# Kernel tuning notes

Measured on AMD Instinct MI355X. Metric: run time of the kernel, lower is better.

## Reference

```python
import jax, jax.numpy as jnp
import numpy as np

B, N, M, D_IN, D_OUT, H = 4, 2048, 2048, 512, 512, 8
HD = D_OUT // H
LN_EPS = 1e-5


def setup_inputs() -> dict:
    key = jax.random.key(0)
    ks = jax.random.split(key, 10)
    query = jax.random.normal(ks[0], (B, N, D_IN), dtype=jnp.float32)
    kee = jax.random.normal(ks[1], (B, M, D_IN), dtype=jnp.float32)
    val = jax.random.normal(ks[2], (B, M, D_IN), dtype=jnp.float32)
    mask = jax.random.randint(ks[3], (B, N, M), 0, 2, dtype=jnp.int32)
    # xavier_uniform with gain 1/sqrt(2): limit = gain * sqrt(6/(fan_in+fan_out))
    lim = (1.0 / np.sqrt(2.0)) * np.sqrt(6.0 / (D_IN + D_OUT))
    WQ = jax.random.uniform(ks[4], (D_OUT, D_IN), jnp.float32, -lim, lim)
    WK = jax.random.uniform(ks[5], (D_OUT, D_IN), jnp.float32, -lim, lim)
    WV = jax.random.uniform(ks[6], (D_OUT, D_IN), jnp.float32, -lim, lim)
    limO = (1.0 / np.sqrt(2.0)) * np.sqrt(6.0 / (D_OUT + D_OUT))
    WO = jax.random.uniform(ks[7], (D_OUT, D_OUT), jnp.float32, -limO, limO)
    bO = jnp.zeros((D_OUT,), jnp.float32)
    gamma = jnp.ones((D_OUT,), jnp.float32)
    beta = jnp.zeros((D_OUT,), jnp.float32)
    return {"query": query, "key": kee, "value": val, "mask": mask,
            "WQ": WQ, "WK": WK, "WV": WV, "WO": WO, "bO": bO,
            "gamma": gamma, "beta": beta}


def reference(query, key, value, mask, WQ, WK, WV, WO, bO, gamma, beta):
    scale = jnp.float32(1.0 / np.sqrt(HD))
    # project and split heads: [B, H, S, HD]
    Q = (query @ WQ.T).reshape(B, N, H, HD).transpose(0, 2, 1, 3)
    K = (key @ WK.T).reshape(B, M, H, HD).transpose(0, 2, 1, 3)
    V = (value @ WV.T).reshape(B, M, H, HD).transpose(0, 2, 1, 3)
    attn = jnp.einsum('bhnd,bhmd->bhnm', Q, K) * scale
    attn = jnp.where(mask[:, None, :, :] == 0, -jnp.inf, attn)
    attn = jax.nn.softmax(attn, axis=-1)  # dropout is identity in eval
    out = jnp.einsum('bhnm,bhmd->bhnd', attn, V)
    out = out.transpose(0, 2, 1, 3).reshape(B, N, D_OUT)
    out = out @ WO.T + bO
    x = out + query  # residual_proj is Identity (input_dim == output_dim)
    mu = jnp.mean(x, axis=-1, keepdims=True)
    var = jnp.var(x, axis=-1, keepdims=True)
    return (x - mu) * jax.lax.rsqrt(var + LN_EPS) * gamma + beta
```

## Files before the change

### kernel.cpp

```cpp
#include <hip/hip_runtime.h>
#include <stdint.h>

#define B_   4
#define N_   2048
#define M_   2048
#define DIN  512
#define DOUT 512
#define H_   8
#define HD_  64
#define ROWS (B_ * N_)

typedef __attribute__((ext_vector_type(8))) short bf16x8;
typedef __attribute__((ext_vector_type(4))) float f32x4;
typedef unsigned short u16;
typedef unsigned int   u32;

__device__ __forceinline__ u16 f2bf(float x) {
  union { float f; u32 u; } v; v.f = x;
  u32 r = (v.u + 0x7FFFu + ((v.u >> 16) & 1u)) >> 16;
  return (u16)r;
}

__device__ __forceinline__ void gld16(u16* lds, const u16* g) {
  __builtin_amdgcn_global_load_lds((const __attribute__((address_space(1))) u32*)g,
                                   (__attribute__((address_space(3))) u32*)lds, 16, 0, 0);
}

__global__ __launch_bounds__(256) void k_convert3(
    const float* __restrict__ a0, const float* __restrict__ a1, const float* __restrict__ a2,
    u16* __restrict__ d0, u16* __restrict__ d1, u16* __restrict__ d2)
{
  int t = blockIdx.x * 256 + threadIdx.x;
  int seg = t >> 19;
  int i = (t & 524287) << 3;
  const float* s = seg == 0 ? a0 : seg == 1 ? a1 : a2;
  u16* d = seg == 0 ? d0 : seg == 1 ? d1 : d2;
  f32x4 x = *(const f32x4*)(s + i);
  f32x4 y = *(const f32x4*)(s + i + 4);
  bf16x8 r;
  r[0] = (short)f2bf(x[0]); r[1] = (short)f2bf(x[1]);
  r[2] = (short)f2bf(x[2]); r[3] = (short)f2bf(x[3]);
  r[4] = (short)f2bf(y[0]); r[5] = (short)f2bf(y[1]);
  r[6] = (short)f2bf(y[2]); r[7] = (short)f2bf(y[3]);
  *(bf16x8*)(d + i) = r;
}

__global__ __launch_bounds__(256) void k_convertw(
    const float* __restrict__ a0, const float* __restrict__ a1,
    const float* __restrict__ a2, const float* __restrict__ a3,
    u16* __restrict__ d0, u16* __restrict__ d1, u16* __restrict__ d2, u16* __restrict__ d3)
{
  int t = blockIdx.x * 256 + threadIdx.x;
  int seg = t >> 15;
  int i = (t & 32767) << 3;
  const float* s = seg == 0 ? a0 : seg == 1 ? a1 : seg == 2 ? a2 : a3;
  u16* d = seg == 0 ? d0 : seg == 1 ? d1 : seg == 2 ? d2 : d3;
  f32x4 x = *(const f32x4*)(s + i);
  f32x4 y = *(const f32x4*)(s + i + 4);
  bf16x8 r;
  r[0] = (short)f2bf(x[0]); r[1] = (short)f2bf(x[1]);
  r[2] = (short)f2bf(x[2]); r[3] = (short)f2bf(x[3]);
  r[4] = (short)f2bf(y[0]); r[5] = (short)f2bf(y[1]);
  r[6] = (short)f2bf(y[2]); r[7] = (short)f2bf(y[3]);
  *(bf16x8*)(d + i) = r;
}

__global__ __launch_bounds__(256) void k_maskpack(const int* __restrict__ mask, u32* __restrict__ bits)
{
  int lane = threadIdx.x & 63;
  int gw = (blockIdx.x * 256 + threadIdx.x) >> 6;
  #pragma unroll 4
  for (int it = 0; it < 32; ++it) {
    long pos = ((long)(it * 8192 + gw)) * 64 + lane;
    int v = mask[pos];
    unsigned long long bal = __ballot(v != 0);
    if ((lane & 31) == 0) bits[pos >> 5] = (u32)(bal >> lane);
  }
}

__global__ __launch_bounds__(256) void k_gemm_qkv(
    const u16* __restrict__ Aq, const u16* __restrict__ Ak, const u16* __restrict__ Av,
    const u16* __restrict__ Wq, const u16* __restrict__ Wk, const u16* __restrict__ Wv,
    u16* __restrict__ Qo, u16* __restrict__ Ko, u16* __restrict__ Vt)
{
  __shared__ __align__(16) u16 At[128 * 64];
  __shared__ __align__(16) u16 Bt[128 * 64];
  const int z = blockIdx.z;
  const u16* A = z == 0 ? Aq : z == 1 ? Ak : Av;
  const u16* W = z == 0 ? Wq : z == 1 ? Wk : Wv;
  const int bm = blockIdx.y, bn = blockIdx.x;
  const int t = threadIdx.x, l = t & 63;
  const int w = t >> 6, wr = w >> 1, wc = w & 1;
  const int l15 = l & 15, lg = l >> 4;
  f32x4 acc[4][4] = {};
  const u16* ga = A + (size_t)(bm * 128 + (t >> 3)) * DIN + (t & 7) * 8;
  const u16* gb = W + (size_t)(bn * 128 + (t >> 3)) * DIN + (t & 7) * 8;
  u16* la = &At[t * 8];
  u16* lb = &Bt[t * 8];
  for (int kt = 0; kt < 8; ++kt) {
    const int k0 = kt * 64;
    #pragma unroll
    for (int s2 = 0; s2 < 4; ++s2) {
      gld16(la + s2 * 2048, ga + (size_t)s2 * 32 * DIN + k0);
      gld16(lb + s2 * 2048, gb + (size_t)s2 * 32 * DIN + k0);
    }
    __syncthreads();
    bf16x8 af[4][2], bfr[4][2];
    #pragma unroll
    for (int mi = 0; mi < 4; ++mi)
      #pragma unroll
      for (int c = 0; c < 2; ++c)
        af[mi][c] = *(const bf16x8*)&At[(wr * 64 + mi * 16 + l15) * 64 + c * 32 + lg * 8];
    #pragma unroll
    for (int ni = 0; ni < 4; ++ni)
      #pragma unroll
      for (int c = 0; c < 2; ++c)
        bfr[ni][c] = *(const bf16x8*)&Bt[(wc * 64 + ni * 16 + l15) * 64 + c * 32 + lg * 8];
    #pragma unroll
    for (int mi = 0; mi < 4; ++mi)
      #pragma unroll
      for (int ni = 0; ni < 4; ++ni) {
        acc[mi][ni] = __builtin_amdgcn_mfma_f32_16x16x32_bf16(af[mi][0], bfr[ni][0], acc[mi][ni], 0, 0, 0);
        acc[mi][ni] = __builtin_amdgcn_mfma_f32_16x16x32_bf16(af[mi][1], bfr[ni][1], acc[mi][ni], 0, 0, 0);
      }
    __syncthreads();
  }
  if (z < 2) {
    u16* C = z == 0 ? Qo : Ko;
    const float scl = z == 0 ? 0.125f : 1.0f;
    #pragma unroll
    for (int mi = 0; mi < 4; ++mi)
      #pragma unroll
      for (int ni = 0; ni < 4; ++ni) {
        const int m = bm * 128 + wr * 64 + mi * 16 + lg * 4;
        const int o = bn * 128 + wc * 64 + ni * 16 + l15;
        #pragma unroll
        for (int r = 0; r < 4; ++r)
          C[(size_t)(m + r) * DOUT + o] = f2bf(acc[mi][ni][r] * scl);
      }
  } else {
    #pragma unroll
    for (int mi = 0; mi < 4; ++mi)
      #pragma unroll
      for (int ni = 0; ni < 4; ++ni) {
        #pragma unroll
        for (int r = 0; r < 4; ++r) {
          const int m = bm * 128 + wr * 64 + mi * 16 + lg * 4 + r;
          const int o = bn * 128 + wc * 64 + ni * 16 + l15;
          const int bb = m >> 11, s = m & 2047;
          Vt[(size_t)(bb * 512 + o) * M_ + s] = f2bf(acc[mi][ni][r]);
        }
      }
  }
}

__global__ __launch_bounds__(256) void k_attn(
    const u16* __restrict__ Qp, const u16* __restrict__ Kp, const u16* __restrict__ Vt,
    const u32* __restrict__ mbits, u16* __restrict__ AO)
{
  __shared__ __align__(16) u16 KT[2][64 * 64];
  __shared__ __align__(16) u16 VT[2][64 * 64];
  const int qt = blockIdx.x, bh = blockIdx.y;
  const int b = bh >> 3, h = bh & 7;
  const int t = threadIdx.x, l = t & 63, w = t >> 6;
  const int l15 = l & 15, lg = l >> 4;

  const int srow = t >> 3;
  const int scol8 = t & 7;
  const int scol = (scol8 ^ (srow & 7)) * 8;
  const int kpr = (srow >> 5) * 32 + (((srow >> 4) & 1) * 4) + (((srow & 15) >> 2) * 8) + (srow & 3);
  const u16* gK = Kp + (size_t)(b * N_ + kpr) * DOUT + h * HD_ + scol;
  const u16* gV = Vt + (size_t)(b * 512 + h * HD_ + srow) * M_ + scol;

  const size_t qglob = (size_t)(b * N_ + qt * 64 + w * 16 + l15);
  const bf16x8 qb0 = *(const bf16x8*)&Qp[qglob * DOUT + h * HD_ + lg * 8];
  const bf16x8 qb1 = *(const bf16x8*)&Qp[qglob * DOUT + h * HD_ + 32 + lg * 8];
  const size_t mrowbase = ((size_t)(b * N_) + qt * 64 + w * 16 + l15) * (M_ / 32);

  f32x4 o0 = {}, o1 = {}, o2 = {}, o3 = {};
  float lsum = 0.f;

  #define STAGE(buf_, m0_) do {                                   \
    const u16* gk_ = gK + (size_t)(m0_) * DOUT;                   \
    const u16* gv_ = gV + (m0_);                                  \
    u16* lk_ = &KT[buf_][t * 8];                                  \
    u16* lv_ = &VT[buf_][t * 8];                                  \
    gld16(lk_, gk_);                                              \
    gld16(lk_ + 2048, gk_ + (size_t)32 * DOUT);                   \
    gld16(lv_, gv_);                                              \
    gld16(lv_ + 2048, gv_ + (size_t)32 * M_);                     \
  } while (0)

  STAGE(0, 0);
  __syncthreads();

  for (int it = 0; it < 32; ++it) {
    const int buf = it & 1;
    const int m0 = it * 64;
    if (it + 1 < 32) STAGE(buf ^ 1, m0 + 64);

    const u32 mw0 = mbits[mrowbase + (m0 >> 5)];
    const u32 mw1 = mbits[mrowbase + (m0 >> 5) + 1];

    const u16* Kb = KT[buf];
    const u16* Vb = VT[buf];

    f32x4 s_[2][2];
    #pragma unroll
    for (int kb = 0; kb < 2; ++kb)
      #pragma unroll
      for (int u = 0; u < 2; ++u) {
        const int row = kb * 32 + u * 16 + l15;
        const bf16x8 a0 = *(const bf16x8*)&Kb[row * 64 + ((lg ^ (row & 7)) * 8)];
        const bf16x8 a1 = *(const bf16x8*)&Kb[row * 64 + (((4 + lg) ^ (row & 7)) * 8)];
        f32x4 z = {};
        z = __builtin_amdgcn_mfma_f32_16x16x32_bf16(a0, qb0, z, 0, 0, 0);
        z = __builtin_amdgcn_mfma_f32_16x16x32_bf16(a1, qb1, z, 0, 0, 0);
        s_[kb][u] = z;
      }

    u32 pk_[2][4];
    #pragma unroll
    for (int kb = 0; kb < 2; ++kb) {
      const u32 mw = kb ? mw1 : mw0;
      float pv[8];
      #pragma unroll
      for (int u = 0; u < 2; ++u)
        #pragma unroll
        for (int r = 0; r < 4; ++r) {
          const int bit = lg * 8 + u * 4 + r;
          float p = __expf(s_[kb][u][r]);
          p = ((mw >> bit) & 1u) ? p : 0.f;
          lsum += p;
          pv[u * 4 + r] = p;
        }
      #pragma unroll
      for (int j = 0; j < 4; ++j) {
        u32 rr;
        asm("v_cvt_pk_bf16_f32 %0, %1, %2" : "=v"(rr) : "v"(pv[2 * j]), "v"(pv[2 * j + 1]));
        pk_[kb][j] = rr;
      }
    }

    union { u32 u[4]; bf16x8 v; } pa0, pa1;
    pa0.u[0] = pk_[0][0]; pa0.u[1] = pk_[0][1]; pa0.u[2] = pk_[0][2]; pa0.u[3] = pk_[0][3];
    pa1.u[0] = pk_[1][0]; pa1.u[1] = pk_[1][1]; pa1.u[2] = pk_[1][2]; pa1.u[3] = pk_[1][3];
    #pragma unroll
    for (int nd = 0; nd < 4; ++nd) {
      const int vrow = nd * 16 + l15;
      const bf16x8 vb0 = *(const bf16x8*)&Vb[vrow * 64 + ((lg ^ (l15 & 7)) * 8)];
      const bf16x8 vb1 = *(const bf16x8*)&Vb[vrow * 64 + (((4 + lg) ^ (l15 & 7)) * 8)];
      f32x4* oo = nd == 0 ? &o0 : nd == 1 ? &o1 : nd == 2 ? &o2 : &o3;
      *oo = __builtin_amdgcn_mfma_f32_16x16x32_bf16(pa0.v, vb0, *oo, 0, 0, 0);
      *oo = __builtin_amdgcn_mfma_f32_16x16x32_bf16(pa1.v, vb1, *oo, 0, 0, 0);
    }
    __syncthreads();
  }

  lsum += __shfl_xor(lsum, 16);
  lsum += __shfl_xor(lsum, 32);
  const float rin = lsum > 0.f ? 1.f / lsum : 0.f;
  float rq[4];
  #pragma unroll
  for (int r = 0; r < 4; ++r) rq[r] = __shfl(rin, lg * 4 + r);
  f32x4* ovec[4] = { &o0, &o1, &o2, &o3 };
  #pragma unroll
  for (int nd = 0; nd < 4; ++nd)
    #pragma unroll
    for (int r = 0; r < 4; ++r) {
      const int q = qt * 64 + w * 16 + lg * 4 + r;
      AO[((size_t)(b * N_ + q)) * DOUT + h * HD_ + nd * 16 + l15] = f2bf((*ovec[nd])[r] * rq[r]);
    }
  #undef STAGE
}

__global__ __launch_bounds__(256) void k_gemm_out(
    const u16* __restrict__ A, const u16* __restrict__ W,
    const float* __restrict__ bO, const float* __restrict__ query,
    float* __restrict__ X)
{
  __shared__ __align__(16) u16 At[128 * 64];
  __shared__ __align__(16) u16 Bt[128 * 64];
  const int bm = blockIdx.y, bn = blockIdx.x;
  const int t = threadIdx.x, l = t & 63;
  const int w = t >> 6, wr = w >> 1, wc = w & 1;
  const int l15 = l & 15, lg = l >> 4;
  f32x4 acc[4][4] = {};
  const u16* ga = A + (size_t)(bm * 128 + (t >> 3)) * DOUT + (t & 7) * 8;
  const u16* gb = W + (size_t)(bn * 128 + (t >> 3)) * DOUT + (t & 7) * 8;
  u16* la = &At[t * 8];
  u16* lb = &Bt[t * 8];
  for (int kt = 0; kt < 8; ++kt) {
    const int k0 = kt * 64;
    #pragma unroll
    for (int s2 = 0; s2 < 4; ++s2) {
      gld16(la + s2 * 2048, ga + (size_t)s2 * 32 * DOUT + k0);
      gld16(lb + s2 * 2048, gb + (size_t)s2 * 32 * DOUT + k0);
    }
    __syncthreads();
    bf16x8 af[4][2], bfr[4][2];
    #pragma unroll
    for (int mi = 0; mi < 4; ++mi)
      #pragma unroll
      for (int c = 0; c < 2; ++c)
        af[mi][c] = *(const bf16x8*)&At[(wr * 64 + mi * 16 + l15) * 64 + c * 32 + lg * 8];
    #pragma unroll
    for (int ni = 0; ni < 4; ++ni)
      #pragma unroll
      for (int c = 0; c < 2; ++c)
        bfr[ni][c] = *(const bf16x8*)&Bt[(wc * 64 + ni * 16 + l15) * 64 + c * 32 + lg * 8];
    #pragma unroll
    for (int mi = 0; mi < 4; ++mi)
      #pragma unroll
      for (int ni = 0; ni < 4; ++ni) {
        acc[mi][ni] = __builtin_amdgcn_mfma_f32_16x16x32_bf16(af[mi][0], bfr[ni][0], acc[mi][ni], 0, 0, 0);
        acc[mi][ni] = __builtin_amdgcn_mfma_f32_16x16x32_bf16(af[mi][1], bfr[ni][1], acc[mi][ni], 0, 0, 0);
      }
    __syncthreads();
  }
  #pragma unroll
  for (int mi = 0; mi < 4; ++mi)
    #pragma unroll
    for (int ni = 0; ni < 4; ++ni) {
      const int m = bm * 128 + wr * 64 + mi * 16 + lg * 4;
      const int o = bn * 128 + wc * 64 + ni * 16 + l15;
      const float bo = bO[o];
      #pragma unroll
      for (int r = 0; r < 4; ++r) {
        const size_t idx = (size_t)(m + r) * DOUT + o;
        X[idx] = acc[mi][ni][r] + bo + query[idx];
      }
    }
}

__global__ __launch_bounds__(256) void k_ln(
    const float* __restrict__ X, const float* __restrict__ gamma,
    const float* __restrict__ beta, float* __restrict__ out)
{
  const int w = threadIdx.x >> 6, l = threadIdx.x & 63;
  const int row = blockIdx.x * 4 + w;
  const float* x = X + (size_t)row * DOUT + l * 8;
  f32x4 a = *(const f32x4*)(x);
  f32x4 b = *(const f32x4*)(x + 4);
  float s = a[0] + a[1] + a[2] + a[3] + b[0] + b[1] + b[2] + b[3];
  float q = a[0]*a[0] + a[1]*a[1] + a[2]*a[2] + a[3]*a[3]
          + b[0]*b[0] + b[1]*b[1] + b[2]*b[2] + b[3]*b[3];
  #pragma unroll
  for (int m = 1; m < 64; m <<= 1) { s += __shfl_xor(s, m); q += __shfl_xor(q, m); }
  const float mean = s * (1.f / 512.f);
  const float var = q * (1.f / 512.f) - mean * mean;
  const float rstd = rsqrtf(var + 1e-5f);
  f32x4 g1 = *(const f32x4*)(gamma + l * 8);
  f32x4 g2 = *(const f32x4*)(gamma + l * 8 + 4);
  f32x4 e1 = *(const f32x4*)(beta + l * 8);
  f32x4 e2 = *(const f32x4*)(beta + l * 8 + 4);
  f32x4 r1, r2;
  #pragma unroll
  for (int i = 0; i < 4; ++i) {
    r1[i] = (a[i] - mean) * rstd * g1[i] + e1[i];
    r2[i] = (b[i] - mean) * rstd * g2[i] + e2[i];
  }
  float* op = out + (size_t)row * DOUT + l * 8;
  *(f32x4*)(op) = r1;
  *(f32x4*)(op + 4) = r2;
}

extern "C" void kernel_launch(void* const* d_in, const int* in_sizes, int n_in,
                              void* d_out, int out_size, void* d_ws, size_t ws_size,
                              hipStream_t stream)
{
  const float* query = (const float*)d_in[0];
  const float* key   = (const float*)d_in[1];
  const float* value = (const float*)d_in[2];
  const int*   mask  = (const int*)d_in[3];
  const float* WQ    = (const float*)d_in[4];
  const float* WK    = (const float*)d_in[5];
  const float* WV    = (const float*)d_in[6];
  const float* WO    = (const float*)d_in[7];
  const float* bO    = (const float*)d_in[8];
  const float* gamma = (const float*)d_in[9];
  const float* beta  = (const float*)d_in[10];
  float* out = (float*)d_out;

  char* ws = (char*)d_ws;
  size_t off = 0;
  auto alloc = [&](size_t bytes) -> char* {
    char* p = ws + off;
    off += (bytes + 255) & ~(size_t)255;
    return p;
  };
  u16* qb  = (u16*)alloc((size_t)ROWS * DIN * 2);
  u16* kb  = (u16*)alloc((size_t)ROWS * DIN * 2);
  u16* vb  = (u16*)alloc((size_t)ROWS * DIN * 2);
  u16* wq  = (u16*)alloc((size_t)DOUT * DIN * 2);
  u16* wk  = (u16*)alloc((size_t)DOUT * DIN * 2);
  u16* wv  = (u16*)alloc((size_t)DOUT * DIN * 2);
  u16* wo  = (u16*)alloc((size_t)DOUT * DIN * 2);
  u16* Qp  = (u16*)alloc((size_t)ROWS * DOUT * 2);
  u16* Kp  = (u16*)alloc((size_t)ROWS * DOUT * 2);
  u16* Vt  = (u16*)alloc((size_t)ROWS * DOUT * 2);
  u32* mb  = (u32*)alloc((size_t)B_ * N_ * (M_ / 32) * 4);
  u16* AO  = (u16*)alloc((size_t)ROWS * DOUT * 2);
  float* X = (float*)alloc((size_t)ROWS * DOUT * 4);

  k_convert3 <<<6144, 256, 0, stream>>>(query, key, value, qb, kb, vb);
  k_convertw <<<512, 256, 0, stream>>>(WQ, WK, WV, WO, wq, wk, wv, wo);
  k_maskpack <<<2048, 256, 0, stream>>>(mask, mb);
  k_gemm_qkv <<<dim3(4, 64, 3), 256, 0, stream>>>(qb, kb, vb, wq, wk, wv, Qp, Kp, Vt);
  k_attn     <<<dim3(32, 32), 256, 0, stream>>>(Qp, Kp, Vt, mb, AO);
  k_gemm_out <<<dim3(4, 64), 256, 0, stream>>>(AO, wo, bO, query, X);
  k_ln       <<<2048, 256, 0, stream>>>(X, gamma, beta, out);
}
```

Baseline: 289.4 us.

## Read int mask directly in attention, merge conversions, double query rows per wave

Drops the separate mask bit-packing kernel. The attention kernel now reads the int32 mask straight from global memory and multiplies the probabilities by it. The two fp32-to-bf16 conversion kernels become a single launch. Each wave now handles 32 query rows instead of 16, so every K/V tile loaded into LDS is reused twice, and the grid is halved. The softmax scale folds in log2(e) so the kernel can use exp2, and row sums are computed with an MFMA against a ones vector instead of scalar adds and shuffles. In exchange, attention reads the full 4-byte-per-element mask (64 MB of mask traffic across all heads) instead of packed bits, and each wave needs more registers.

New measurement: 287.4 us. Within noise of the previous version (-0.7%).

```diff
diff --git a/kernel.cpp b/kernel.cpp
--- a/kernel.cpp
+++ b/kernel.cpp
@@ -15,6 +15,12 @@
 typedef unsigned short u16;
 typedef unsigned int   u32;
 
+#if __has_builtin(__builtin_amdgcn_exp2f)
+#define EXP2(x) __builtin_amdgcn_exp2f(x)
+#else
+#define EXP2(x) exp2f(x)
+#endif
+
 __device__ __forceinline__ u16 f2bf(float x) {
   union { float f; u32 u; } v; v.f = x;
   u32 r = (v.u + 0x7FFFu + ((v.u >> 16) & 1u)) >> 16;
@@ -26,15 +32,27 @@
                                    (__attribute__((address_space(3))) u32*)lds, 16, 0, 0);
 }
 
-__global__ __launch_bounds__(256) void k_convert3(
-    const float* __restrict__ a0, const float* __restrict__ a1, const float* __restrict__ a2,
-    u16* __restrict__ d0, u16* __restrict__ d1, u16* __restrict__ d2)
-{
-  int t = blockIdx.x * 256 + threadIdx.x;
-  int seg = t >> 19;
-  int i = (t & 524287) << 3;
-  const float* s = seg == 0 ? a0 : seg == 1 ? a1 : a2;
-  u16* d = seg == 0 ? d0 : seg == 1 ? d1 : d2;
+__global__ __launch_bounds__(256) void k_prep(
+    const float* __restrict__ q, const float* __restrict__ k, const float* __restrict__ v,
+    const float* __restrict__ wq_, const float* __restrict__ wk_,
+    const float* __restrict__ wv_, const float* __restrict__ wo_,
+    u16* __restrict__ qb, u16* __restrict__ kb, u16* __restrict__ vb,
+    u16* __restrict__ wqb, u16* __restrict__ wkb, u16* __restrict__ wvb, u16* __restrict__ wob)
+{
+  const int id = blockIdx.x;
+  const float* s; u16* d; size_t i;
+  if (id < 6144) {
+    const int seg = id >> 11;
+    s = seg == 0 ? q : seg == 1 ? k : v;
+    d = seg == 0 ? qb : seg == 1 ? kb : vb;
+    i = (size_t)(id & 2047) * 2048 + threadIdx.x * 8;
+  } else {
+    const int wid = id - 6144;
+    const int seg = wid >> 7;
+    s = seg == 0 ? wq_ : seg == 1 ? wk_ : seg == 2 ? wv_ : wo_;
+    d = seg == 0 ? wqb : seg == 1 ? wkb : seg == 2 ? wvb : wob;
+    i = (size_t)(wid & 127) * 2048 + threadIdx.x * 8;
+  }
   f32x4 x = *(const f32x4*)(s + i);
   f32x4 y = *(const f32x4*)(s + i + 4);
   bf16x8 r;
@@ -43,39 +61,6 @@
   r[4] = (short)f2bf(y[0]); r[5] = (short)f2bf(y[1]);
   r[6] = (short)f2bf(y[2]); r[7] = (short)f2bf(y[3]);
   *(bf16x8*)(d + i) = r;
-}
-
-__global__ __launch_bounds__(256) void k_convertw(
-    const float* __restrict__ a0, const float* __restrict__ a1,
-    const float* __restrict__ a2, const float* __restrict__ a3,
-    u16* __restrict__ d0, u16* __restrict__ d1, u16* __restrict__ d2, u16* __restrict__ d3)
-{
-  int t = blockIdx.x * 256 + threadIdx.x;
-  int seg = t >> 15;
-  int i = (t & 32767) << 3;
-  const float* s = seg == 0 ? a0 : seg == 1 ? a1 : seg == 2 ? a2 : a3;
-  u16* d = seg == 0 ? d0 : seg == 1 ? d1 : seg == 2 ? d2 : d3;
-  f32x4 x = *(const f32x4*)(s + i);
-  f32x4 y = *(const f32x4*)(s + i + 4);
-  bf16x8 r;
-  r[0] = (short)f2bf(x[0]); r[1] = (short)f2bf(x[1]);
-  r[2] = (short)f2bf(x[2]); r[3] = (short)f2bf(x[3]);
-  r[4] = (short)f2bf(y[0]); r[5] = (short)f2bf(y[1]);
-  r[6] = (short)f2bf(y[2]); r[7] = (short)f2bf(y[3]);
-  *(bf16x8*)(d + i) = r;
-}
-
-__global__ __launch_bounds__(256) void k_maskpack(const int* __restrict__ mask, u32* __restrict__ bits)
-{
-  int lane = threadIdx.x & 63;
-  int gw = (blockIdx.x * 256 + threadIdx.x) >> 6;
-  #pragma unroll 4
-  for (int it = 0; it < 32; ++it) {
-    long pos = ((long)(it * 8192 + gw)) * 64 + lane;
-    int v = mask[pos];
-    unsigned long long bal = __ballot(v != 0);
-    if ((lane & 31) == 0) bits[pos >> 5] = (u32)(bal >> lane);
-  }
 }
 
 __global__ __launch_bounds__(256) void k_gemm_qkv(
@@ -127,7 +112,7 @@
   }
   if (z < 2) {
     u16* C = z == 0 ? Qo : Ko;
-    const float scl = z == 0 ? 0.125f : 1.0f;
+    const float scl = z == 0 ? 0.18033688f : 1.0f;
     #pragma unroll
     for (int mi = 0; mi < 4; ++mi)
       #pragma unroll
@@ -156,7 +141,7 @@
 
 __global__ __launch_bounds__(256) void k_attn(
     const u16* __restrict__ Qp, const u16* __restrict__ Kp, const u16* __restrict__ Vt,
-    const u32* __restrict__ mbits, u16* __restrict__ AO)
+    const int* __restrict__ mask, u16* __restrict__ AO)
 {
   __shared__ __align__(16) u16 KT[2][64 * 64];
   __shared__ __align__(16) u16 VT[2][64 * 64];
@@ -172,13 +157,22 @@
   const u16* gK = Kp + (size_t)(b * N_ + kpr) * DOUT + h * HD_ + scol;
   const u16* gV = Vt + (size_t)(b * 512 + h * HD_ + srow) * M_ + scol;
 
-  const size_t qglob = (size_t)(b * N_ + qt * 64 + w * 16 + l15);
-  const bf16x8 qb0 = *(const bf16x8*)&Qp[qglob * DOUT + h * HD_ + lg * 8];
-  const bf16x8 qb1 = *(const bf16x8*)&Qp[qglob * DOUT + h * HD_ + 32 + lg * 8];
-  const size_t mrowbase = ((size_t)(b * N_) + qt * 64 + w * 16 + l15) * (M_ / 32);
-
-  f32x4 o0 = {}, o1 = {}, o2 = {}, o3 = {};
-  float lsum = 0.f;
+  const int qrow0 = qt * 128 + w * 32 + l15;
+  const bf16x8 qf[2][2] = {
+    { *(const bf16x8*)&Qp[((size_t)(b * N_) + qrow0) * DOUT + h * HD_ + lg * 8],
+      *(const bf16x8*)&Qp[((size_t)(b * N_) + qrow0) * DOUT + h * HD_ + 32 + lg * 8] },
+    { *(const bf16x8*)&Qp[((size_t)(b * N_) + qrow0 + 16) * DOUT + h * HD_ + lg * 8],
+      *(const bf16x8*)&Qp[((size_t)(b * N_) + qrow0 + 16) * DOUT + h * HD_ + 32 + lg * 8] } };
+
+  const int* mk[2] = { mask + ((size_t)(b * N_) + qrow0) * M_ + lg * 8,
+                       mask + ((size_t)(b * N_) + qrow0 + 16) * M_ + lg * 8 };
+
+  f32x4 o[2][4] = {};
+  f32x4 lacc[2] = {};
+
+  union U8 { u32 u[4]; bf16x8 v; };
+  U8 ones;
+  ones.u[0] = ones.u[1] = ones.u[2] = ones.u[3] = 0x3F803F80u;
 
   #define STAGE(buf_, m0_) do {                                   \
     const u16* gk_ = gK + (size_t)(m0_) * DOUT;                   \
@@ -199,78 +193,86 @@
     const int m0 = it * 64;
     if (it + 1 < 32) STAGE(buf ^ 1, m0 + 64);
 
-    const u32 mw0 = mbits[mrowbase + (m0 >> 5)];
-    const u32 mw1 = mbits[mrowbase + (m0 >> 5) + 1];
-
     const u16* Kb = KT[buf];
     const u16* Vb = VT[buf];
-
-    f32x4 s_[2][2];
+    const int xs = l15 & 7;
+
+    bf16x8 ka[2][2][2];
     #pragma unroll
     for (int kb = 0; kb < 2; ++kb)
       #pragma unroll
       for (int u = 0; u < 2; ++u) {
         const int row = kb * 32 + u * 16 + l15;
-        const bf16x8 a0 = *(const bf16x8*)&Kb[row * 64 + ((lg ^ (row & 7)) * 8)];
-        const bf16x8 a1 = *(const bf16x8*)&Kb[row * 64 + (((4 + lg) ^ (row & 7)) * 8)];
-        f32x4 z = {};
-        z = __builtin_amdgcn_mfma_f32_16x16x32_bf16(a0, qb0, z, 0, 0, 0);
-        z = __builtin_amdgcn_mfma_f32_16x16x32_bf16(a1, qb1, z, 0, 0, 0);
-        s_[kb][u] = z;
-      }
-
-    u32 pk_[2][4];
-    #pragma unroll
-    for (int kb = 0; kb < 2; ++kb) {
-      const u32 mw = kb ? mw1 : mw0;
-      float pv[8];
-      #pragma unroll
-      for (int u = 0; u < 2; ++u)
+        ka[kb][u][0] = *(const bf16x8*)&Kb[row * 64 + ((lg ^ xs) * 8)];
+        ka[kb][u][1] = *(const bf16x8*)&Kb[row * 64 + (((4 + lg) ^ xs) * 8)];
+      }
+
+    U8 pa[2][2];
+    #pragma unroll
+    for (int s = 0; s < 2; ++s) {
+      f32x4 sS[2][2];
+      #pragma unroll
+      for (int kb = 0; kb < 2; ++kb)
         #pragma unroll
-        for (int r = 0; r < 4; ++r) {
-          const int bit = lg * 8 + u * 4 + r;
-          float p = __expf(s_[kb][u][r]);
-          p = ((mw >> bit) & 1u) ? p : 0.f;
-          lsum += p;
-          pv[u * 4 + r] = p;
+        for (int u = 0; u < 2; ++u) {
+          f32x4 z = {};
+          z = __builtin_amdgcn_mfma_f32_16x16x32_bf16(ka[kb][u][0], qf[s][0], z, 0, 0, 0);
+          z = __builtin_amdgcn_mfma_f32_16x16x32_bf16(ka[kb][u][1], qf[s][1], z, 0, 0, 0);
+          sS[kb][u] = z;
         }
       #pragma unroll
-      for (int j = 0; j < 4; ++j) {
-        u32 rr;
-        asm("v_cvt_pk_bf16_f32 %0, %1, %2" : "=v"(rr) : "v"(pv[2 * j]), "v"(pv[2 * j + 1]));
-        pk_[kb][j] = rr;
-      }
-    }
-
-    union { u32 u[4]; bf16x8 v; } pa0, pa1;
-    pa0.u[0] = pk_[0][0]; pa0.u[1] = pk_[0][1]; pa0.u[2] = pk_[0][2]; pa0.u[3] = pk_[0][3];
-    pa1.u[0] = pk_[1][0]; pa1.u[1] = pk_[1][1]; pa1.u[2] = pk_[1][2]; pa1.u[3] = pk_[1][3];
+      for (int kb = 0; kb < 2; ++kb) {
+        const int4 ma  = *(const int4*)(mk[s] + m0 + kb * 32);
+        const int4 mb2 = *(const int4*)(mk[s] + m0 + kb * 32 + 4);
+        float e[8];
+        #pragma unroll
+        for (int u = 0; u < 2; ++u)
+          #pragma unroll
+          for (int r = 0; r < 4; ++r)
+            e[u * 4 + r] = EXP2(sS[kb][u][r]);
+        e[0] *= (float)ma.x;  e[1] *= (float)ma.y;  e[2] *= (float)ma.z;  e[3] *= (float)ma.w;
+        e[4] *= (float)mb2.x; e[5] *= (float)mb2.y; e[6] *= (float)mb2.z; e[7] *= (float)mb2.w;
+        #pragma unroll
+        for (int j = 0; j < 4; ++j) {
+          u32 rr;
+          asm("v_cvt_pk_bf16_f32 %0, %1, %2" : "=v"(rr) : "v"(e[2 * j]), "v"(e[2 * j + 1]));
+          pa[s][kb].u[j] = rr;
+        }
+      }
+      lacc[s] = __builtin_amdgcn_mfma_f32_16x16x32_bf16(pa[s][0].v, ones.v, lacc[s], 0, 0, 0);
+      lacc[s] = __builtin_amdgcn_mfma_f32_16x16x32_bf16(pa[s][1].v, ones.v, lacc[s], 0, 0, 0);
+    }
+
     #pragma unroll
     for (int nd = 0; nd < 4; ++nd) {
       const int vrow = nd * 16 + l15;
-      const bf16x8 vb0 = *(const bf16x8*)&Vb[vrow * 64 + ((lg ^ (l15 & 7)) * 8)];
-      const bf16x8 vb1 = *(const bf16x8*)&Vb[vrow * 64 + (((4 + lg) ^ (l15 & 7)) * 8)];
-      f32x4* oo = nd == 0 ? &o0 : nd == 1 ? &o1 : nd == 2 ? &o2 : &o3;
-      *oo = __builtin_amdgcn_mfma_f32_16x16x32_bf16(pa0.v, vb0, *oo, 0, 0, 0);
-      *oo = __builtin_amdgcn_mfma_f32_16x16x32_bf16(pa1.v, vb1, *oo, 0, 0, 0);
+      const bf16x8 vb0 = *(const bf16x8*)&Vb[vrow * 64 + ((lg ^ xs) * 8)];
+      const bf16x8 vb1 = *(const bf16x8*)&Vb[vrow * 64 + (((4 + lg) ^ xs) * 8)];
+      #pragma unroll
+      for (int s = 0; s < 2; ++s) {
+        o[s][nd] = __builtin_amdgcn_mfma_f32_16x16x32_bf16(pa[s][0].v, vb0, o[s][nd], 0, 0, 0);
+        o[s][nd] = __builtin_amdgcn_mfma_f32_16x16x32_bf16(pa[s][1].v, vb1, o[s][nd], 0, 0, 0);
+      }
     }
     __syncthreads();
   }
 
-  lsum += __shfl_xor(lsum, 16);
-  lsum += __shfl_xor(lsum, 32);
-  const float rin = lsum > 0.f ? 1.f / lsum : 0.f;
-  float rq[4];
   #pragma unroll
-  for (int r = 0; r < 4; ++r) rq[r] = __shfl(rin, lg * 4 + r);
-  f32x4* ovec[4] = { &o0, &o1, &o2, &o3 };
-  #pragma unroll
-  for (int nd = 0; nd < 4; ++nd)
+  for (int s = 0; s < 2; ++s) {
+    float rq[4];
     #pragma unroll
     for (int r = 0; r < 4; ++r) {
-      const int q = qt * 64 + w * 16 + lg * 4 + r;
-      AO[((size_t)(b * N_ + q)) * DOUT + h * HD_ + nd * 16 + l15] = f2bf((*ovec[nd])[r] * rq[r]);
-    }
+      const float ls = lacc[s][r];
+      rq[r] = ls > 0.f ? 1.f / ls : 0.f;
+    }
+    #pragma unroll
+    for (int nd = 0; nd < 4; ++nd)
+      #pragma unroll
+      for (int r = 0; r < 4; ++r) {
+        const int q = qt * 128 + w * 32 + s * 16 + lg * 4 + r;
+        AO[((size_t)(b * N_ + q)) * DOUT + h * HD_ + nd * 16 + l15] = f2bf(o[s][nd][r] * rq[r]);
+      }
+  }
   #undef STAGE
 }
 
@@ -399,15 +401,13 @@
   u16* Qp  = (u16*)alloc((size_t)ROWS * DOUT * 2);
   u16* Kp  = (u16*)alloc((size_t)ROWS * DOUT * 2);
   u16* Vt  = (u16*)alloc((size_t)ROWS * DOUT * 2);
-  u32* mb  = (u32*)alloc((size_t)B_ * N_ * (M_ / 32) * 4);
   u16* AO  = (u16*)alloc((size_t)ROWS * DOUT * 2);
   float* X = (float*)alloc((size_t)ROWS * DOUT * 4);
 
-  k_convert3 <<<6144, 256, 0, stream>>>(query, key, value, qb, kb, vb);
-  k_convertw <<<512, 256, 0, stream>>>(WQ, WK, WV, WO, wq, wk, wv, wo);
-  k_maskpack <<<2048, 256, 0, stream>>>(mask, mb);
+  k_prep     <<<6656, 256, 0, stream>>>(query, key, value, WQ, WK, WV, WO,
+                                        qb, kb, vb, wq, wk, wv, wo);
   k_gemm_qkv <<<dim3(4, 64, 3), 256, 0, stream>>>(qb, kb, vb, wq, wk, wv, Qp, Kp, Vt);
-  k_attn     <<<dim3(32, 32), 256, 0, stream>>>(Qp, Kp, Vt, mb, AO);
+  k_attn     <<<dim3(16, 32), 256, 0, stream>>>(Qp, Kp, Vt, mask, AO);
   k_gemm_out <<<dim3(4, 64), 256, 0, stream>>>(AO, wo, bO, query, X);
   k_ln       <<<2048, 256, 0, stream>>>(X, gamma, beta, out);
 }
```
